# Performance work log

Hardware: AMD Instinct MI355X
Metric: run time of the kernel (lower is better)

The kernel has to match this reference:

```python
import jax, jax.numpy as jnp
import numpy as np

# Module config (matches init_kwargs)
RADIUS = 1
N_POINTS = 8
NUM_BINS = 8
DENSITY = True
LBP_MAX = 2 ** N_POINTS - 1  # 255


def _circle_offsets(radius, n_points):
    # skimage local_binary_pattern sampling coordinates:
    # rr = -radius*sin(2*pi*i/P), cc = radius*cos(2*pi*i/P)
    offs = []
    for i in range(n_points):
        ang = 2.0 * np.pi * i / n_points
        dy = -radius * np.sin(ang)
        dx = radius * np.cos(ang)
        # skimage snaps near-integer coords to exact integers (eps rounding)
        if abs(dy - round(dy)) < 1e-8:
            dy = float(round(dy))
        if abs(dx - round(dx)) < 1e-8:
            dx = float(round(dx))
        offs.append((dy, dx))
    return offs


def _bilinear_shift(xp, pad, dy, dx, H, W):
    # Bilinear sample of every pixel's neighbor at constant offset (dy, dx),
    # zero padding outside the image (skimage uses constant-0 border mode).
    fy, fx = int(np.floor(dy)), int(np.floor(dx))
    ty, tx = dy - fy, dx - fx

    def sl(oy, ox):
        return xp[..., pad + oy:pad + oy + H, pad + ox:pad + ox + W]

    return ((1.0 - ty) * (1.0 - tx) * sl(fy, fx)
            + (1.0 - ty) * tx * sl(fy, fx + 1)
            + ty * (1.0 - tx) * sl(fy + 1, fx)
            + ty * tx * sl(fy + 1, fx + 1))


def _lbp_codes(x):
    # x: (B, C, H, W) -> integer-valued LBP codes (B, C, H, W), method='default'
    B, C, H, W = x.shape
    pad = int(np.ceil(RADIUS)) + 1
    xp = jnp.pad(x, ((0, 0), (0, 0), (pad, pad), (pad, pad)))
    code = jnp.zeros(x.shape, dtype=jnp.float32)
    for i, (dy, dx) in enumerate(_circle_offsets(RADIUS, N_POINTS)):
        nb = _bilinear_shift(xp, pad, dy, dx, H, W)
        bit = (nb - x >= 0).astype(jnp.float32)
        code = code + bit * float(2 ** i)
    return code


def _histogram(codes):
    # np.histogram(bins=NUM_BINS, range=(0, LBP_MAX), density=True) per channel
    B, C, H, W = codes.shape
    width = LBP_MAX / NUM_BINS
    idx = jnp.clip((codes * (1.0 / width)).astype(jnp.int32), 0, NUM_BINS - 1)
    idx_flat = idx.reshape(B * C, H * W)
    counts = jax.vmap(
        lambda ix: jnp.zeros((NUM_BINS,), jnp.float32).at[ix].add(1.0)
    )(idx_flat)  # (B*C, NUM_BINS)
    if DENSITY:
        counts = counts / (float(H * W) * width)
    return counts.reshape(B, C, NUM_BINS)


def setup_inputs() -> dict:
    key = jax.random.key(0)
    x = jax.random.normal(key, (32, 3, 512, 512), dtype=jnp.float32)
    return {"x": x}


def reference(x):
    codes = _lbp_codes(x)               # (B, C, H, W)
    hist = _histogram(codes)            # (B, C, NUM_BINS)
    return hist.reshape(hist.shape[0], -1).astype(jnp.float32)  # (B, C*NUM_BINS)
```

## Files before the change

kernel.cpp:

```cpp
#include <hip/hip_runtime.h>

#define W 512
#define H 512
#define CH_PIX (W * H)
#define NCH 96

__global__ __launch_bounds__(768) void zero_out_k(unsigned int* out) {
    int i = threadIdx.x;
    if (i < 768) out[i] = 0u;
}

__global__ __launch_bounds__(256) void lbp_main_k(const float* __restrict__ x,
                                                  unsigned int* __restrict__ gc) {
    const int chan = blockIdx.x;
    const int band = blockIdx.y;
    const int tid  = threadIdx.x;
    const int g     = tid & 127;
    const int strip = tid >> 7;
    const int lane  = tid & 63;

    __shared__ unsigned int h[8 * 64];
    for (int i = tid; i < 512; i += 256) h[i] = 0u;
    __syncthreads();

    constexpr double Sd = 0.7071067811865476;
    constexpr double Td = 1.0 - Sd;
    const float wSS = (float)(Sd * Sd);
    const float wST = (float)(Sd * Td);
    const float wTT = (float)(Td * Td);

    const int  col  = g << 2;
    const bool g0   = (g == 0), g127 = (g == 127);

    if (band < 16) {
        const int y0   = band * 32 + strip * 16;
        const int yend = min(y0 + 16, 511);

        int idx = chan * CH_PIX + y0 * W + col;
        float4 m4 = *(const float4*)(x + idx);
        float  mL = g0   ? 0.0f : x[idx - 1];
        float  mR = g127 ? 0.0f : x[idx + 4];

        for (int y = y0; y < yend; ++y) {
            const int idxD = idx + W;
            float4 d4 = *(const float4*)(x + idxD);
            float  dL = g0   ? 0.0f : x[idxD - 1];
            float  dR = g127 ? 0.0f : x[idxD + 4];

            const float cs[4]  = {m4.x, m4.y, m4.z, m4.w};
            const float es[4]  = {m4.y, m4.z, m4.w, mR};
            const float ws[4]  = {mL,   m4.x, m4.y, m4.z};
            const float ss[4]  = {d4.x, d4.y, d4.z, d4.w};
            const float sws[4] = {dL,   d4.x, d4.y, d4.z};
            const float ses[4] = {d4.y, d4.z, d4.w, dR};

            #pragma unroll
            for (int i = 0; i < 4; ++i) {
                const float c  = cs[i];
                const float tc = wTT * c;
                const float ts = wST * ss[i];
                const float nb5 = ((wST * ws[i] + tc) + wSS * sws[i]) + ts;
                const float nb7 = ((tc + wST * es[i]) + ts) + wSS * ses[i];
                const int bin = (nb5 >= c ? 1 : 0) | (ss[i] >= c ? 2 : 0) |
                                (nb7 >= c ? 4 : 0);
                atomicAdd(&h[(bin << 6) + lane], 1u);
            }
            m4 = d4; mL = dL; mR = dR;
            idx = idxD;
        }
    } else if (strip == 0) {
        const int idx = chan * CH_PIX + 511 * W + col;
        float4 m4 = *(const float4*)(x + idx);
        float  mL = g0   ? 0.0f : x[idx - 1];
        float  mR = g127 ? 0.0f : x[idx + 4];

        const float cs[4] = {m4.x, m4.y, m4.z, m4.w};
        const float es[4] = {m4.y, m4.z, m4.w, mR};
        const float ws[4] = {mL,   m4.x, m4.y, m4.z};

        #pragma unroll
        for (int i = 0; i < 4; ++i) {
            const float c  = cs[i];
            const float tc = wTT * c;
            const float ts = wST * 0.0f;
            const float nb5 = ((wST * ws[i] + tc) + wSS * 0.0f) + ts;
            const float nb7 = ((tc + wST * es[i]) + ts) + wSS * 0.0f;
            const int bin = (nb5 >= c ? 1 : 0) | (0.0f >= c ? 2 : 0) |
                            (nb7 >= c ? 4 : 0);
            atomicAdd(&h[(bin << 6) + lane], 1u);
        }
    }
    __syncthreads();

    if (tid < 8) {
        unsigned int s = 0;
        #pragma unroll
        for (int l = 0; l < 64; ++l) s += h[(tid << 6) + l];
        atomicAdd(&gc[chan * 8 + tid], s);
    }
}

__global__ __launch_bounds__(768) void finalize_k(unsigned int* io) {
    int i = threadIdx.x;
    if (i < 768) {
        unsigned int u = io[i];
        ((float*)io)[i] = (float)u / 8355840.0f;
    }
}

extern "C" void kernel_launch(void* const* d_in, const int* in_sizes, int n_in,
                              void* d_out, int out_size, void* d_ws, size_t ws_size,
                              hipStream_t stream) {
    const float* x = (const float*)d_in[0];
    unsigned int* out = (unsigned int*)d_out;

    zero_out_k<<<1, 768, 0, stream>>>(out);
    dim3 grid(NCH, 17);
    lbp_main_k<<<grid, 256, 0, stream>>>(x, out);
    finalize_k<<<1, 768, 0, stream>>>(out);
}
```

Before: 30.71 us.

## Pack per-thread bin counts into 64-bit register and drop global atomics

Each thread now accumulates its 8 bin counts as packed bytes in a single 64-bit register instead of issuing a shared-memory atomic per pixel, then does 8 shared atomics at the end. All 17 rows per thread are loaded up front into registers for memory-level parallelism. Global atomics and the zeroing kernel are replaced by per-block partials in workspace reduced by the finalize kernel, removing one launch. The costs are higher register pressure from 17 float4 rows and a byte-field overflow risk, which holds only because each thread handles at most 64 pixels.

```diff
diff --git a/kernel.cpp b/kernel.cpp
--- a/kernel.cpp
+++ b/kernel.cpp
@@ -3,15 +3,9 @@
 #define W 512
 #define H 512
 #define CH_PIX (W * H)
-#define NCH 96
-
-__global__ __launch_bounds__(768) void zero_out_k(unsigned int* out) {
-    int i = threadIdx.x;
-    if (i < 768) out[i] = 0u;
-}
 
 __global__ __launch_bounds__(256) void lbp_main_k(const float* __restrict__ x,
-                                                  unsigned int* __restrict__ gc) {
+                                                  unsigned int* __restrict__ ws) {
     const int chan = blockIdx.x;
     const int band = blockIdx.y;
     const int tid  = threadIdx.x;
@@ -32,63 +26,81 @@
     const int  col  = g << 2;
     const bool g0   = (g == 0), g127 = (g == 127);
 
+    unsigned long long c64 = 0ull;
+
     if (band < 16) {
-        const int y0   = band * 32 + strip * 16;
-        const int yend = min(y0 + 16, 511);
+        const int y0 = band * 32 + strip * 16;
+        const int nr = (y0 == 496) ? 15 : 16;
+        const int base = chan * CH_PIX + y0 * W + col;
 
-        int idx = chan * CH_PIX + y0 * W + col;
-        float4 m4 = *(const float4*)(x + idx);
-        float  mL = g0   ? 0.0f : x[idx - 1];
-        float  mR = g127 ? 0.0f : x[idx + 4];
+        float4 r4[17];
+        float  rL[17], rR[17];
+        #pragma unroll
+        for (int k = 0; k < 17; ++k) {
+            const int kk   = (y0 + k > 511) ? (511 - y0) : k;
+            const int ridx = base + kk * W;
+            r4[k] = *(const float4*)(x + ridx);
+            rL[k] = g0   ? 0.0f : x[ridx - 1];
+            rR[k] = g127 ? 0.0f : x[ridx + 4];
+        }
 
-        for (int y = y0; y < yend; ++y) {
-            const int idxD = idx + W;
-            float4 d4 = *(const float4*)(x + idxD);
-            float  dL = g0   ? 0.0f : x[idxD - 1];
-            float  dR = g127 ? 0.0f : x[idxD + 4];
+        #pragma unroll
+        for (int k = 0; k < 16; ++k) {
+            if (k < nr) {
+                const float4 m4 = r4[k], d4 = r4[k + 1];
+                const float mL = rL[k], mR = rR[k];
+                const float dL = rL[k + 1], dR = rR[k + 1];
 
-            const float cs[4]  = {m4.x, m4.y, m4.z, m4.w};
-            const float es[4]  = {m4.y, m4.z, m4.w, mR};
-            const float ws[4]  = {mL,   m4.x, m4.y, m4.z};
-            const float ss[4]  = {d4.x, d4.y, d4.z, d4.w};
-            const float sws[4] = {dL,   d4.x, d4.y, d4.z};
-            const float ses[4] = {d4.y, d4.z, d4.w, dR};
+                const float cs[4]  = {m4.x, m4.y, m4.z, m4.w};
+                const float es[4]  = {m4.y, m4.z, m4.w, mR};
+                const float wsA[4] = {mL,   m4.x, m4.y, m4.z};
+                const float ss[4]  = {d4.x, d4.y, d4.z, d4.w};
+                const float sws[4] = {dL,   d4.x, d4.y, d4.z};
+                const float ses[4] = {d4.y, d4.z, d4.w, dR};
 
-            #pragma unroll
-            for (int i = 0; i < 4; ++i) {
-                const float c  = cs[i];
-                const float tc = wTT * c;
-                const float ts = wST * ss[i];
-                const float nb5 = ((wST * ws[i] + tc) + wSS * sws[i]) + ts;
-                const float nb7 = ((tc + wST * es[i]) + ts) + wSS * ses[i];
-                const int bin = (nb5 >= c ? 1 : 0) | (ss[i] >= c ? 2 : 0) |
-                                (nb7 >= c ? 4 : 0);
-                atomicAdd(&h[(bin << 6) + lane], 1u);
+                #pragma unroll
+                for (int i = 0; i < 4; ++i) {
+                    const float c  = cs[i];
+                    const float tc = wTT * c;
+                    const float ts = wST * ss[i];
+                    const float nb5 = ((wST * wsA[i] + tc) + wSS * sws[i]) + ts;
+                    const float nb7 = ((tc + wST * es[i]) + ts) + wSS * ses[i];
+                    const unsigned int amt = (nb5   >= c ? 8u  : 0u)
+                                           + (ss[i] >= c ? 16u : 0u)
+                                           + (nb7   >= c ? 32u : 0u);
+                    c64 += 1ull << amt;
+                }
             }
-            m4 = d4; mL = dL; mR = dR;
-            idx = idxD;
         }
     } else if (strip == 0) {
         const int idx = chan * CH_PIX + 511 * W + col;
-        float4 m4 = *(const float4*)(x + idx);
-        float  mL = g0   ? 0.0f : x[idx - 1];
-        float  mR = g127 ? 0.0f : x[idx + 4];
+        const float4 m4 = *(const float4*)(x + idx);
+        const float mL = g0   ? 0.0f : x[idx - 1];
+        const float mR = g127 ? 0.0f : x[idx + 4];
 
-        const float cs[4] = {m4.x, m4.y, m4.z, m4.w};
-        const float es[4] = {m4.y, m4.z, m4.w, mR};
-        const float ws[4] = {mL,   m4.x, m4.y, m4.z};
+        const float cs[4]  = {m4.x, m4.y, m4.z, m4.w};
+        const float es[4]  = {m4.y, m4.z, m4.w, mR};
+        const float wsA[4] = {mL,   m4.x, m4.y, m4.z};
 
         #pragma unroll
         for (int i = 0; i < 4; ++i) {
             const float c  = cs[i];
             const float tc = wTT * c;
-            const float ts = wST * 0.0f;
-            const float nb5 = ((wST * ws[i] + tc) + wSS * 0.0f) + ts;
-            const float nb7 = ((tc + wST * es[i]) + ts) + wSS * 0.0f;
-            const int bin = (nb5 >= c ? 1 : 0) | (0.0f >= c ? 2 : 0) |
-                            (nb7 >= c ? 4 : 0);
-            atomicAdd(&h[(bin << 6) + lane], 1u);
+            const float nb5 = ((wST * wsA[i] + tc) + wSS * 0.0f) + wST * 0.0f;
+            const float nb7 = ((tc + wST * es[i]) + wST * 0.0f) + wSS * 0.0f;
+            const unsigned int amt = (nb5  >= c ? 8u  : 0u)
+                                   + (0.0f >= c ? 16u : 0u)
+                                   + (nb7  >= c ? 32u : 0u);
+            c64 += 1ull << amt;
         }
+    }
+
+    const unsigned int lo = (unsigned int)c64;
+    const unsigned int hi = (unsigned int)(c64 >> 32);
+    #pragma unroll
+    for (int b = 0; b < 4; ++b) {
+        atomicAdd(&h[(b       << 6) + lane], (lo >> (b * 8)) & 0xffu);
+        atomicAdd(&h[((b + 4) << 6) + lane], (hi >> (b * 8)) & 0xffu);
     }
     __syncthreads();
 
@@ -96,15 +108,19 @@
         unsigned int s = 0;
         #pragma unroll
         for (int l = 0; l < 64; ++l) s += h[(tid << 6) + l];
-        atomicAdd(&gc[chan * 8 + tid], s);
+        ws[(chan * 17 + band) * 8 + tid] = s;
     }
 }
 
-__global__ __launch_bounds__(768) void finalize_k(unsigned int* io) {
-    int i = threadIdx.x;
-    if (i < 768) {
-        unsigned int u = io[i];
-        ((float*)io)[i] = (float)u / 8355840.0f;
+__global__ __launch_bounds__(64) void finalize_k(const unsigned int* __restrict__ ws,
+                                                 float* __restrict__ out) {
+    const int gid = blockIdx.x * 64 + threadIdx.x;
+    if (gid < 768) {
+        const int chan = gid >> 3, bin = gid & 7;
+        unsigned int s = 0;
+        #pragma unroll
+        for (int b = 0; b < 17; ++b) s += ws[(chan * 17 + b) * 8 + bin];
+        out[gid] = (float)s / 8355840.0f;
     }
 }
 
@@ -112,10 +128,10 @@
                               void* d_out, int out_size, void* d_ws, size_t ws_size,
                               hipStream_t stream) {
     const float* x = (const float*)d_in[0];
-    unsigned int* out = (unsigned int*)d_out;
+    unsigned int* wsp = (unsigned int*)d_ws;
+    float* out = (float*)d_out;
 
-    zero_out_k<<<1, 768, 0, stream>>>(out);
-    dim3 grid(NCH, 17);
-    lbp_main_k<<<grid, 256, 0, stream>>>(x, out);
-    finalize_k<<<1, 768, 0, stream>>>(out);
+    dim3 grid(96, 17);
+    lbp_main_k<<<grid, 256, 0, stream>>>(x, wsp);
+    finalize_k<<<12, 64, 0, stream>>>(wsp, out);
 }
```

Measured after the change: 28.42 us. -7.5%, faster.
